# Kernel optimization log

Measured on AMD Instinct MI355X. Metric: run time of the kernel, lower is better.

## Reference

```python
import jax, jax.numpy as jnp
import numpy as np

B, S, NK, H, D, DM = 2, 2048, 32, 8, 64, 512
NEG = -1e9


def setup_inputs() -> dict:
    key = jax.random.key(0)
    ks = jax.random.split(key, 12)
    hidden_states = jax.random.normal(ks[0], (B, S, DM), jnp.float32)
    rpe = jax.random.normal(ks[1], (B, S, NK, H), jnp.float32)
    idx = jax.random.randint(ks[2], (S, NK), 0, S)
    pad = jax.random.uniform(ks[3], (S, NK)) < 0.1
    q_k_mask = jnp.where(pad, -1, idx).astype(jnp.int32)
    k_q_mask = jax.random.randint(ks[4], (S, NK), 0, S).astype(jnp.int32)  # only used by TVM backward
    sc = 0.02
    w_q = jax.random.normal(ks[5], (DM, H * D), jnp.float32) * sc
    w_k = jax.random.normal(ks[6], (DM, H * D), jnp.float32) * sc
    w_v = jax.random.normal(ks[7], (DM, H * D), jnp.float32) * sc
    fc_w = jax.random.normal(ks[8], (H * D, DM), jnp.float32) * sc
    fc_b = jnp.zeros((DM,), jnp.float32)
    ln_g = jnp.ones((DM,), jnp.float32)
    ln_b = jnp.zeros((DM,), jnp.float32)
    return {"hidden_states": hidden_states, "rpe": rpe, "q_k_mask": q_k_mask,
            "k_q_mask": k_q_mask, "w_q": w_q, "w_k": w_k, "w_v": w_v,
            "fc_w": fc_w, "fc_b": fc_b, "ln_g": ln_g, "ln_b": ln_b}


def reference(hidden_states, rpe, q_k_mask, k_q_mask, w_q, w_k, w_v, fc_w, fc_b, ln_g, ln_b):
    bsz, seq_len, _ = hidden_states.shape
    q = (hidden_states @ w_q).reshape(bsz, seq_len, H, D)
    k = (hidden_states @ w_k).reshape(bsz, seq_len, H, D)
    v = (hidden_states @ w_v).reshape(bsz, seq_len, H, D)

    valid = q_k_mask >= 0                      # [S, NK]
    idx = jnp.where(valid, q_k_mask, 0)        # safe gather index
    vmask = valid[None, :, None, :]            # [1,S,1,NK] broadcast over (b, h)

    # QKP_mm_tvm: sparse QK^T over neighbor lists, plus relative-position bias,
    # padded slots -> -1e9.  k_g: [B,S,NK,H,D]
    k_g = k[:, idx]
    scores = jnp.einsum('bshd,bsnhd->bshn', q, k_g) + rpe.transpose(0, 1, 3, 2)
    scores = jnp.where(vmask, scores, NEG)
    scores = scores / (D ** 0.5)

    attn = jax.nn.softmax(scores, axis=-1)
    # AttnV_mm_tvm with padding 0: padded slots contribute nothing.
    attn = attn * vmask
    v_g = v[:, idx]                            # [B,S,NK,H,D]
    ctx = jnp.einsum('bshn,bsnhd->bshd', attn, v_g).reshape(bsz, seq_len, H * D)

    out = ctx @ fc_w + fc_b + hidden_states    # dropout = identity (eval)
    mu = jnp.mean(out, axis=-1, keepdims=True)
    var = jnp.mean((out - mu) ** 2, axis=-1, keepdims=True)
    return (out - mu) * jax.lax.rsqrt(var + 1e-6) * ln_g + ln_b
```

## Files before the change

kernel.cpp:

```cpp
#include <hip/hip_runtime.h>
#include <hip/hip_bf16.h>

constexpr int Bb  = 2;
constexpr int Ss  = 2048;
constexpr int NKk = 32;
constexpr int Hh  = 8;
constexpr int DMm = 512;
constexpr int Mm  = Bb * Ss;
constexpr int QKV = 1536;

typedef __attribute__((ext_vector_type(8))) short bf16x8;
typedef __attribute__((ext_vector_type(4))) float f32x4;

__device__ __forceinline__ float b2f(unsigned short u) {
  return __uint_as_float((unsigned)u << 16);
}
__device__ __forceinline__ unsigned short f2b(float f) {
  unsigned u = __float_as_uint(f);
  unsigned r = (u + 0x7fffu + ((u >> 16) & 1u)) >> 16;
  return (unsigned short)r;
}
__device__ __forceinline__ void gload_lds16(const ushort* g, ushort* l) {
  __builtin_amdgcn_global_load_lds(
      (const __attribute__((address_space(1))) void*)g,
      (__attribute__((address_space(3))) void*)l, 16, 0, 0);
}

__global__ __launch_bounds__(256) void cvt_all_k(
    const float* __restrict__ hs,
    const float* __restrict__ Wq, const float* __restrict__ Wk,
    const float* __restrict__ Wv, const float* __restrict__ Wf,
    ushort* __restrict__ Xb, ushort* __restrict__ Wt3, ushort* __restrict__ Wtf)
{
  __shared__ float tile[64][65];
  const int z = blockIdx.z;
  const int t = threadIdx.x;

  if (z >= 4) {
    const int cid = (z - 4) * 64 + blockIdx.x * 8 + blockIdx.y;
    const size_t base8 = (size_t)cid * 1024;
#pragma unroll
    for (int it = 0; it < 4; ++it) {
      const size_t i = base8 + it * 256 + t;
      const float4 a = reinterpret_cast<const float4*>(hs)[2 * i];
      const float4 b = reinterpret_cast<const float4*>(hs)[2 * i + 1];
      ushort o[8] = {f2b(a.x), f2b(a.y), f2b(a.z), f2b(a.w),
                     f2b(b.x), f2b(b.y), f2b(b.z), f2b(b.w)};
      reinterpret_cast<uint4*>(Xb)[i] = *reinterpret_cast<uint4*>(o);
    }
    return;
  }

  const float* W = (z == 0) ? Wq : (z == 1) ? Wk : (z == 2) ? Wv : Wf;
  ushort* Wt = (z < 3) ? (Wt3 + (size_t)z * 512 * 512) : Wtf;

  const int k0 = blockIdx.x * 64, n0 = blockIdx.y * 64;
#pragma unroll
  for (int p = 0; p < 4; ++p) {
    const int r = (t >> 4) + p * 16, c = (t & 15) * 4;
    const float4 v = *reinterpret_cast<const float4*>(&W[(size_t)(k0 + r) * 512 + n0 + c]);
    tile[r][c] = v.x; tile[r][c + 1] = v.y; tile[r][c + 2] = v.z; tile[r][c + 3] = v.w;
  }
  __syncthreads();
  const int n = t >> 2, ks = (t & 3) * 16;
  ushort o[16];
#pragma unroll
  for (int i = 0; i < 16; ++i) o[i] = f2b(tile[ks + i][n]);
  *reinterpret_cast<uint4*>(&Wt[(size_t)(n0 + n) * 512 + k0 + ks])     = *reinterpret_cast<uint4*>(&o[0]);
  *reinterpret_cast<uint4*>(&Wt[(size_t)(n0 + n) * 512 + k0 + ks + 8]) = *reinterpret_cast<uint4*>(&o[8]);
}

template <int OUT_BF16, int BMv, int BNv>
__global__ __launch_bounds__(256) void gemm_pipe(
    const ushort* __restrict__ Xb, const ushort* __restrict__ Wt,
    void* __restrict__ Yv, const float* __restrict__ bias,
    const float* __restrict__ resid, int ldY)
{
  constexpr int MI  = BMv / 32;
  constexpr int NJ  = BNv / 32;
  constexpr int STG = MI + NJ;
  constexpr int ASZ = BMv * 64;
  __shared__ ushort smem[2 * ASZ + 2 * BNv * 64];

  const int bm = blockIdx.x * BMv;
  const int bn = blockIdx.y * BNv;
  const int t  = threadIdx.x;
  const int wave = t >> 6, lane = t & 63;
  const int wm = (wave >> 1) * (BMv / 2);
  const int wn = (wave & 1) * (BNv / 2);

  f32x4 acc[MI][NJ] = {};

  auto stage = [&](int buf, int k0) {
    ushort* A = smem + buf * ASZ;
    ushort* B = smem + 2 * ASZ + buf * (BNv * 64);
#pragma unroll
    for (int p = 0; p < MI; ++p) {
      const int i = p * 256 + t;
      const int row = i >> 3, sb = i & 7;
      gload_lds16(Xb + (size_t)(bm + row) * 512 + k0 + ((sb ^ (row & 7)) << 3),
                  &A[(size_t)(p * 256 + wave * 64) * 8]);
    }
#pragma unroll
    for (int p = 0; p < NJ; ++p) {
      const int i = p * 256 + t;
      const int row = i >> 3, sb = i & 7;
      gload_lds16(Wt + (size_t)(bn + row) * 512 + k0 + ((sb ^ (row & 7)) << 3),
                  &B[(size_t)(p * 256 + wave * 64) * 8]);
    }
  };

  auto compute = [&](int buf) {
    const ushort* A = smem + buf * ASZ;
    const ushort* B = smem + 2 * ASZ + buf * (BNv * 64);
#pragma unroll
    for (int ks = 0; ks < 2; ++ks) {
      const int kb = ks * 4 + (lane >> 4);
      bf16x8 af[MI], bfr[NJ];
#pragma unroll
      for (int i = 0; i < MI; ++i) {
        const int row = wm + i * 16 + (lane & 15);
        af[i] = *reinterpret_cast<const bf16x8*>(&A[row * 64 + ((kb ^ (row & 7)) << 3)]);
      }
#pragma unroll
      for (int j = 0; j < NJ; ++j) {
        const int row = wn + j * 16 + (lane & 15);
        bfr[j] = *reinterpret_cast<const bf16x8*>(&B[row * 64 + ((kb ^ (row & 7)) << 3)]);
      }
#pragma unroll
      for (int i = 0; i < MI; ++i)
#pragma unroll
        for (int j = 0; j < NJ; ++j)
          acc[i][j] = __builtin_amdgcn_mfma_f32_16x16x32_bf16(af[i], bfr[j], acc[i][j], 0, 0, 0);
    }
  };

  stage(0, 0);
  int cur = 0;
#pragma unroll
  for (int i = 0; i < 8; ++i) {
    if (i < 7) {
      stage(cur ^ 1, (i + 1) * 64);
      asm volatile("s_waitcnt vmcnt(%0)" :: "n"(STG) : "memory");
    } else {
      asm volatile("s_waitcnt vmcnt(0)" ::: "memory");
    }
    __builtin_amdgcn_sched_barrier(0);
    __builtin_amdgcn_s_barrier();
    compute(cur);
    __builtin_amdgcn_sched_barrier(0);
    __builtin_amdgcn_s_barrier();
    cur ^= 1;
  }

  if (OUT_BF16) {
#pragma unroll
    for (int i = 0; i < MI; ++i)
#pragma unroll
      for (int j = 0; j < NJ; ++j)
#pragma unroll
        for (int r = 0; r < 4; ++r) {
          const int row = wm + i * 16 + (lane >> 4) * 4 + r;
          const int col = wn + j * 16 + (lane & 15);
          smem[row * BNv + col] = f2b(acc[i][j][r]);
        }
    __syncthreads();
    ushort* Y = reinterpret_cast<ushort*>(Yv);
    constexpr int CPT = BMv * BNv / 8 / 256;
#pragma unroll
    for (int p = 0; p < CPT; ++p) {
      const int c = p * 256 + t;
      const int row = c / (BNv / 8);
      const int cb  = c % (BNv / 8);
      *reinterpret_cast<uint4*>(&Y[(size_t)(bm + row) * ldY + bn + cb * 8]) =
          *reinterpret_cast<uint4*>(&smem[row * BNv + cb * 8]);
    }
  } else {
    float* Y = reinterpret_cast<float*>(Yv);
#pragma unroll
    for (int i = 0; i < MI; ++i) {
#pragma unroll
      for (int j = 0; j < NJ; ++j) {
        const int m = bm + wm + i * 16 + (lane >> 4) * 4;
        const int n = bn + wn + j * 16 + (lane & 15);
        const float bb = bias[n];
#pragma unroll
        for (int r = 0; r < 4; ++r)
          Y[(size_t)(m + r) * ldY + n] = acc[i][j][r] + bb + resid[(size_t)(m + r) * 512 + n];
      }
    }
  }
}

__global__ __launch_bounds__(256) void attn_k6(
    const ushort* __restrict__ qkv, const float* __restrict__ rpe,
    const int* __restrict__ qkm, ushort* __restrict__ ctx)
{
  __shared__ ushort Ks[32 * 512];
  __shared__ float  qs[512];

  const int bs = blockIdx.x;
  const int b  = bs >> 11;
  const int s  = bs & 2047;
  const int t  = threadIdx.x;
  const int wv = t >> 6, lane = t & 63;

  const ushort* qrow = qkv + (size_t)bs * QKV;
  qs[t]       = b2f(qrow[t]);
  qs[t + 256] = b2f(qrow[t + 256]);

#pragma unroll
  for (int r = 0; r < 8; ++r) {
    const int n = r * 4 + wv;
    int im = qkm[s * NKk + n];
    im = im < 0 ? 0 : im;
    const ushort* gsrc = qkv + (size_t)(b * Ss + im) * QKV + 512
                       + ((lane ^ (n & 7)) * 8);
    gload_lds16(gsrc, &Ks[n * 512]);
  }

  const int iv = qkm[s * NKk + (lane & 31)];
  const float rv = rpe[((size_t)bs * NKk + (t & 31)) * Hh + (t >> 5)];

  __syncthreads();

  const ushort* vbase = qkv + (size_t)b * Ss * QKV + 1024;
  const int e = 2 * t;
  uint vvu[32];
#pragma unroll
  for (int n2 = 0; n2 < 32; ++n2) {
    int row = __shfl(iv, (lane & 32) + n2, 64);
    row = row < 0 ? 0 : row;
    vvu[n2] = *reinterpret_cast<const uint*>(&vbase[(size_t)row * QKV + (e & 511)]);
  }

  const int h = t >> 5;
  const int n = t & 31;
  const bool valid = (iv >= 0);

  float2 a2 = make_float2(0.f, 0.f);
#pragma unroll
  for (int j = 0; j < 8; ++j) {
    const int blk = (h * 8 + j) ^ (n & 7);
    const uint4 kk = *reinterpret_cast<const uint4*>(&Ks[n * 512 + blk * 8]);
    const float4 qa = *reinterpret_cast<const float4*>(&qs[h * 64 + j * 8]);
    const float4 qb = *reinterpret_cast<const float4*>(&qs[h * 64 + j * 8 + 4]);
    a2.x += qa.x * __uint_as_float(kk.x << 16);
    a2.y += qa.y * __uint_as_float(kk.x & 0xffff0000u);
    a2.x += qa.z * __uint_as_float(kk.y << 16);
    a2.y += qa.w * __uint_as_float(kk.y & 0xffff0000u);
    a2.x += qb.x * __uint_as_float(kk.z << 16);
    a2.y += qb.y * __uint_as_float(kk.z & 0xffff0000u);
    a2.x += qb.z * __uint_as_float(kk.w << 16);
    a2.y += qb.w * __uint_as_float(kk.w & 0xffff0000u);
  }
  float sc = a2.x + a2.y + rv;
  sc = valid ? sc * 0.125f : -1e30f;

  float mx = sc;
#pragma unroll
  for (int m = 16; m >= 1; m >>= 1) mx = fmaxf(mx, __shfl_xor(mx, m, 32));
  const float p = valid ? __expf(sc - mx) : 0.f;
  float sum = p;
#pragma unroll
  for (int m = 16; m >= 1; m >>= 1) sum += __shfl_xor(sum, m, 32);
  const float pn = (sum > 0.f) ? (p / sum) : 0.f;

  float c0 = 0.f, c1 = 0.f;
#pragma unroll
  for (int n2 = 0; n2 < 32; ++n2) {
    const float a = __shfl(pn, (lane & 32) + n2, 64);
    c0 += a * __uint_as_float(vvu[n2] << 16);
    c1 += a * __uint_as_float(vvu[n2] & 0xffff0000u);
  }
  const uint packed = (uint)f2b(c0) | ((uint)f2b(c1) << 16);
  *reinterpret_cast<uint*>(&ctx[(size_t)bs * 512 + e]) = packed;
}

__global__ __launch_bounds__(256) void ln_k(
    float* __restrict__ x, const float* __restrict__ g,
    const float* __restrict__ bta)
{
  const int w    = threadIdx.x >> 6;
  const int lane = threadIdx.x & 63;
  const int row  = blockIdx.x * 4 + w;

  float4* xr = reinterpret_cast<float4*>(x + (size_t)row * 512);
  const float4 v0 = xr[lane];
  const float4 v1 = xr[lane + 64];

  float sum = v0.x + v0.y + v0.z + v0.w + v1.x + v1.y + v1.z + v1.w;
  float sq  = v0.x * v0.x + v0.y * v0.y + v0.z * v0.z + v0.w * v0.w
            + v1.x * v1.x + v1.y * v1.y + v1.z * v1.z + v1.w * v1.w;
#pragma unroll
  for (int m = 32; m >= 1; m >>= 1) {
    sum += __shfl_xor(sum, m, 64);
    sq  += __shfl_xor(sq,  m, 64);
  }
  const float mu  = sum * (1.f / 512.f);
  const float var = sq * (1.f / 512.f) - mu * mu;
  const float rs  = rsqrtf(var + 1e-6f);

  const float4 g0 = reinterpret_cast<const float4*>(g)[lane];
  const float4 g1 = reinterpret_cast<const float4*>(g)[lane + 64];
  const float4 b0 = reinterpret_cast<const float4*>(bta)[lane];
  const float4 b1 = reinterpret_cast<const float4*>(bta)[lane + 64];

  float4 o0, o1;
  o0.x = (v0.x - mu) * rs * g0.x + b0.x;
  o0.y = (v0.y - mu) * rs * g0.y + b0.y;
  o0.z = (v0.z - mu) * rs * g0.z + b0.z;
  o0.w = (v0.w - mu) * rs * g0.w + b0.w;
  o1.x = (v1.x - mu) * rs * g1.x + b1.x;
  o1.y = (v1.y - mu) * rs * g1.y + b1.y;
  o1.z = (v1.z - mu) * rs * g1.z + b1.z;
  o1.w = (v1.w - mu) * rs * g1.w + b1.w;
  xr[lane]      = o0;
  xr[lane + 64] = o1;
}

extern "C" void kernel_launch(void* const* d_in, const int* in_sizes, int n_in,
                              void* d_out, int out_size, void* d_ws, size_t ws_size,
                              hipStream_t stream) {
  const float* hs  = (const float*)d_in[0];
  const float* rpe = (const float*)d_in[1];
  const int*   qkm = (const int*)d_in[2];
  const float* wq  = (const float*)d_in[4];
  const float* wk  = (const float*)d_in[5];
  const float* wv  = (const float*)d_in[6];
  const float* fcw = (const float*)d_in[7];
  const float* fcb = (const float*)d_in[8];
  const float* lng = (const float*)d_in[9];
  const float* lnb = (const float*)d_in[10];
  float* out = (float*)d_out;

  ushort* Xb  = (ushort*)d_ws;
  ushort* Wt3 = Xb  + (size_t)Mm * DMm;
  ushort* Wtf = Wt3 + (size_t)3 * DMm * DMm;
  ushort* qkv = Wtf + (size_t)DMm * DMm;
  ushort* cxb = qkv + (size_t)Mm * QKV;

  cvt_all_k<<<dim3(8, 8, 8), 256, 0, stream>>>(hs, wq, wk, wv, fcw, Xb, Wt3, Wtf);

  gemm_pipe<1, 128, 96><<<dim3(Mm / 128, QKV / 96), 256, 0, stream>>>(
      Xb, Wt3, qkv, nullptr, nullptr, QKV);

  attn_k6<<<Mm, 256, 0, stream>>>(qkv, rpe, qkm, cxb);

  gemm_pipe<0, 128, 64><<<dim3(Mm / 128, DMm / 64), 256, 0, stream>>>(
      cxb, Wtf, out, fcb, hs, DMm);
  ln_k<<<Mm / 4, 256, 0, stream>>>(out, lng, lnb);
}
```

Baseline: 55.38 us.

## Fuse output projection GEMM with bias, residual and LayerNorm in one kernel

Replaces the fp32-output FC GEMM and the separate LayerNorm kernel with one kernel. Each block computes a 16-row by 512-column tile of ctx@fc_w with MFMA, adds bias and residual into LDS, then normalises each full row and writes the final output. This drops one kernel launch and the fp32 write and re-read of the intermediate. In exchange each block re-streams the whole fc weight matrix, only 256 blocks are launched, and the K-step is small (32), so each block does little work per barrier.

Result: slower. 62.64 us (+13.1%).

```diff
diff --git a/kernel.cpp b/kernel.cpp
--- a/kernel.cpp
+++ b/kernel.cpp
@@ -70,11 +70,10 @@
   *reinterpret_cast<uint4*>(&Wt[(size_t)(n0 + n) * 512 + k0 + ks + 8]) = *reinterpret_cast<uint4*>(&o[8]);
 }
 
-template <int OUT_BF16, int BMv, int BNv>
+template <int BMv, int BNv>
 __global__ __launch_bounds__(256) void gemm_pipe(
     const ushort* __restrict__ Xb, const ushort* __restrict__ Wt,
-    void* __restrict__ Yv, const float* __restrict__ bias,
-    const float* __restrict__ resid, int ldY)
+    ushort* __restrict__ Y, int ldY)
 {
   constexpr int MI  = BMv / 32;
   constexpr int NJ  = BNv / 32;
@@ -153,42 +152,25 @@
     cur ^= 1;
   }
 
-  if (OUT_BF16) {
-#pragma unroll
-    for (int i = 0; i < MI; ++i)
-#pragma unroll
-      for (int j = 0; j < NJ; ++j)
-#pragma unroll
-        for (int r = 0; r < 4; ++r) {
-          const int row = wm + i * 16 + (lane >> 4) * 4 + r;
-          const int col = wn + j * 16 + (lane & 15);
-          smem[row * BNv + col] = f2b(acc[i][j][r]);
-        }
-    __syncthreads();
-    ushort* Y = reinterpret_cast<ushort*>(Yv);
-    constexpr int CPT = BMv * BNv / 8 / 256;
-#pragma unroll
-    for (int p = 0; p < CPT; ++p) {
-      const int c = p * 256 + t;
-      const int row = c / (BNv / 8);
-      const int cb  = c % (BNv / 8);
-      *reinterpret_cast<uint4*>(&Y[(size_t)(bm + row) * ldY + bn + cb * 8]) =
-          *reinterpret_cast<uint4*>(&smem[row * BNv + cb * 8]);
-    }
-  } else {
-    float* Y = reinterpret_cast<float*>(Yv);
-#pragma unroll
-    for (int i = 0; i < MI; ++i) {
-#pragma unroll
-      for (int j = 0; j < NJ; ++j) {
-        const int m = bm + wm + i * 16 + (lane >> 4) * 4;
-        const int n = bn + wn + j * 16 + (lane & 15);
-        const float bb = bias[n];
-#pragma unroll
-        for (int r = 0; r < 4; ++r)
-          Y[(size_t)(m + r) * ldY + n] = acc[i][j][r] + bb + resid[(size_t)(m + r) * 512 + n];
+#pragma unroll
+  for (int i = 0; i < MI; ++i)
+#pragma unroll
+    for (int j = 0; j < NJ; ++j)
+#pragma unroll
+      for (int r = 0; r < 4; ++r) {
+        const int row = wm + i * 16 + (lane >> 4) * 4 + r;
+        const int col = wn + j * 16 + (lane & 15);
+        smem[row * BNv + col] = f2b(acc[i][j][r]);
       }
-    }
+  __syncthreads();
+  constexpr int CPT = BMv * BNv / 8 / 256;
+#pragma unroll
+  for (int p = 0; p < CPT; ++p) {
+    const int c = p * 256 + t;
+    const int row = c / (BNv / 8);
+    const int cb  = c % (BNv / 8);
+    *reinterpret_cast<uint4*>(&Y[(size_t)(bm + row) * ldY + bn + cb * 8]) =
+        *reinterpret_cast<uint4*>(&smem[row * BNv + cb * 8]);
   }
 }
 
@@ -277,46 +259,112 @@
   *reinterpret_cast<uint*>(&ctx[(size_t)bs * 512 + e]) = packed;
 }
 
-__global__ __launch_bounds__(256) void ln_k(
-    float* __restrict__ x, const float* __restrict__ g,
-    const float* __restrict__ bta)
+__global__ __launch_bounds__(256) void fc_ln_k(
+    const ushort* __restrict__ Xc, const ushort* __restrict__ Wtf,
+    float* __restrict__ out, const float* __restrict__ bias,
+    const float* __restrict__ resid,
+    const float* __restrict__ lng, const float* __restrict__ lnb)
 {
-  const int w    = threadIdx.x >> 6;
-  const int lane = threadIdx.x & 63;
-  const int row  = blockIdx.x * 4 + w;
-
-  float4* xr = reinterpret_cast<float4*>(x + (size_t)row * 512);
-  const float4 v0 = xr[lane];
-  const float4 v1 = xr[lane + 64];
-
-  float sum = v0.x + v0.y + v0.z + v0.w + v1.x + v1.y + v1.z + v1.w;
-  float sq  = v0.x * v0.x + v0.y * v0.y + v0.z * v0.z + v0.w * v0.w
-            + v1.x * v1.x + v1.y * v1.y + v1.z * v1.z + v1.w * v1.w;
-#pragma unroll
-  for (int m = 32; m >= 1; m >>= 1) {
-    sum += __shfl_xor(sum, m, 64);
-    sq  += __shfl_xor(sq,  m, 64);
-  }
-  const float mu  = sum * (1.f / 512.f);
-  const float var = sq * (1.f / 512.f) - mu * mu;
-  const float rs  = rsqrtf(var + 1e-6f);
-
-  const float4 g0 = reinterpret_cast<const float4*>(g)[lane];
-  const float4 g1 = reinterpret_cast<const float4*>(g)[lane + 64];
-  const float4 b0 = reinterpret_cast<const float4*>(bta)[lane];
-  const float4 b1 = reinterpret_cast<const float4*>(bta)[lane + 64];
-
-  float4 o0, o1;
-  o0.x = (v0.x - mu) * rs * g0.x + b0.x;
-  o0.y = (v0.y - mu) * rs * g0.y + b0.y;
-  o0.z = (v0.z - mu) * rs * g0.z + b0.z;
-  o0.w = (v0.w - mu) * rs * g0.w + b0.w;
-  o1.x = (v1.x - mu) * rs * g1.x + b1.x;
-  o1.y = (v1.y - mu) * rs * g1.y + b1.y;
-  o1.z = (v1.z - mu) * rs * g1.z + b1.z;
-  o1.w = (v1.w - mu) * rs * g1.w + b1.w;
-  xr[lane]      = o0;
-  xr[lane + 64] = o1;
+  __shared__ ushort Bs[2][512][4][8];
+  __shared__ ushort As[2][16][4][8];
+
+  const int bm = blockIdx.x * 16;
+  const int t  = threadIdx.x;
+  const int wv = t >> 6, lane = t & 63;
+
+  f32x4 acc[8] = {};
+
+  auto stage = [&](int buf, int k0) {
+#pragma unroll
+    for (int p = 0; p < 8; ++p) {
+      const int i = p * 256 + t;
+      const int rn = i >> 2, kb = i & 3;
+      gload_lds16(Wtf + (size_t)rn * 512 + k0 + kb * 8,
+                  &Bs[buf][0][0][0] + (size_t)(p * 256 + wv * 64) * 8);
+    }
+    {
+      const int row = lane >> 2, kb = lane & 3;
+      gload_lds16(Xc + (size_t)(bm + row) * 512 + k0 + kb * 8,
+                  &As[buf][0][0][0]);
+    }
+  };
+
+  auto compute = [&](int buf) {
+    const int kb = lane >> 4, r16 = lane & 15;
+    const bf16x8 af = *reinterpret_cast<const bf16x8*>(&As[buf][r16][kb][0]);
+#pragma unroll
+    for (int j = 0; j < 8; ++j) {
+      const int rn = wv * 128 + j * 16 + r16;
+      const bf16x8 bf = *reinterpret_cast<const bf16x8*>(&Bs[buf][rn][kb][0]);
+      acc[j] = __builtin_amdgcn_mfma_f32_16x16x32_bf16(af, bf, acc[j], 0, 0, 0);
+    }
+  };
+
+  stage(0, 0);
+  int cur = 0;
+#pragma unroll
+  for (int i = 0; i < 16; ++i) {
+    if (i < 15) {
+      stage(cur ^ 1, (i + 1) * 32);
+      asm volatile("s_waitcnt vmcnt(9)" ::: "memory");
+    } else {
+      asm volatile("s_waitcnt vmcnt(0)" ::: "memory");
+    }
+    __builtin_amdgcn_sched_barrier(0);
+    __builtin_amdgcn_s_barrier();
+    compute(cur);
+    __builtin_amdgcn_sched_barrier(0);
+    __builtin_amdgcn_s_barrier();
+    cur ^= 1;
+  }
+
+  float* T = reinterpret_cast<float*>(&Bs[0][0][0][0]);
+  const int r4 = lane >> 4, cn = lane & 15;
+#pragma unroll
+  for (int j = 0; j < 8; ++j) {
+    const int col = wv * 128 + j * 16 + cn;
+    const float bb = bias[col];
+#pragma unroll
+    for (int r = 0; r < 4; ++r) {
+      const int row = r4 * 4 + r;
+      T[row * 516 + col] = acc[j][r] + bb + resid[(size_t)(bm + row) * 512 + col];
+    }
+  }
+  __syncthreads();
+
+#pragma unroll
+  for (int rr = 0; rr < 4; ++rr) {
+    const int row = wv * 4 + rr;
+    const float4 v0 = *reinterpret_cast<const float4*>(&T[row * 516 + lane * 4]);
+    const float4 v1 = *reinterpret_cast<const float4*>(&T[row * 516 + 256 + lane * 4]);
+    float sum = v0.x + v0.y + v0.z + v0.w + v1.x + v1.y + v1.z + v1.w;
+    float sq  = v0.x * v0.x + v0.y * v0.y + v0.z * v0.z + v0.w * v0.w
+              + v1.x * v1.x + v1.y * v1.y + v1.z * v1.z + v1.w * v1.w;
+#pragma unroll
+    for (int m = 32; m >= 1; m >>= 1) {
+      sum += __shfl_xor(sum, m, 64);
+      sq  += __shfl_xor(sq,  m, 64);
+    }
+    const float mu  = sum * (1.f / 512.f);
+    const float var = sq * (1.f / 512.f) - mu * mu;
+    const float rs  = rsqrtf(var + 1e-6f);
+    const float4 g0 = reinterpret_cast<const float4*>(lng)[lane];
+    const float4 g1 = reinterpret_cast<const float4*>(lng)[lane + 64];
+    const float4 b0 = reinterpret_cast<const float4*>(lnb)[lane];
+    const float4 b1 = reinterpret_cast<const float4*>(lnb)[lane + 64];
+    float4 o0, o1;
+    o0.x = (v0.x - mu) * rs * g0.x + b0.x;
+    o0.y = (v0.y - mu) * rs * g0.y + b0.y;
+    o0.z = (v0.z - mu) * rs * g0.z + b0.z;
+    o0.w = (v0.w - mu) * rs * g0.w + b0.w;
+    o1.x = (v1.x - mu) * rs * g1.x + b1.x;
+    o1.y = (v1.y - mu) * rs * g1.y + b1.y;
+    o1.z = (v1.z - mu) * rs * g1.z + b1.z;
+    o1.w = (v1.w - mu) * rs * g1.w + b1.w;
+    float4* orow = reinterpret_cast<float4*>(out + (size_t)(bm + row) * 512);
+    orow[lane]      = o0;
+    orow[lane + 64] = o1;
+  }
 }
 
 extern "C" void kernel_launch(void* const* d_in, const int* in_sizes, int n_in,
@@ -342,12 +390,10 @@
 
   cvt_all_k<<<dim3(8, 8, 8), 256, 0, stream>>>(hs, wq, wk, wv, fcw, Xb, Wt3, Wtf);
 
-  gemm_pipe<1, 128, 96><<<dim3(Mm / 128, QKV / 96), 256, 0, stream>>>(
-      Xb, Wt3, qkv, nullptr, nullptr, QKV);
+  gemm_pipe<128, 96><<<dim3(Mm / 128, QKV / 96), 256, 0, stream>>>(
+      Xb, Wt3, qkv, QKV);
 
   attn_k6<<<Mm, 256, 0, stream>>>(qkv, rpe, qkm, cxb);
 
-  gemm_pipe<0, 128, 64><<<dim3(Mm / 128, DMm / 64), 256, 0, stream>>>(
-      cxb, Wtf, out, fcb, hs, DMm);
-  ln_k<<<Mm / 4, 256, 0, stream>>>(out, lng, lnb);
-}
+  fc_ln_k<<<Mm / 16, 256, 0, stream>>>(cxb, Wtf, out, fcb, hs, lng, lnb);
+}
```
